# Optimization experiments

Measured on AMD Instinct MI355X. Metric: run time of the kernel, lower is better.

Reference implementation:

```python
import jax, jax.numpy as jnp
import numpy as np

EPS_RMS = 1e-6   # assumed eps for utils.rms
EPS_LN = 1e-5    # matches F.layer_norm eps in LayerNorm


def rmsnorm(z):
    # utils.rms: normalize to unit RMS over the channel dim
    return z * jax.lax.rsqrt(jnp.mean(jnp.square(z), axis=-1, keepdims=True) + EPS_RMS)


def layernorm(x, w):
    mu = jnp.mean(x, axis=-1, keepdims=True)
    var = jnp.var(x, axis=-1, keepdims=True)
    return (x - mu) * jax.lax.rsqrt(var + EPS_LN) * w


def polar_orthogonal(W):
    # utils.fast_polar_decomposition: orthogonal factor of polar decomposition
    U, _, Vh = jnp.linalg.svd(W, full_matrices=False)
    return U @ Vh


def pscan2(q, P1, P2, identity):
    # Hillis-Steele inclusive parallel scan over the time axis with combine
    # scan(left, right) = rms(left @ P1^T + right @ P2^T); positions with no
    # left operand at a level keep their current value (identity pads the shift).
    B, T, C = q.shape
    d = 1
    while d < T:
        left = jnp.concatenate(
            [jnp.broadcast_to(identity, (B, d, C)), q[:, : T - d]], axis=1)
        z = rmsnorm(jnp.einsum('btc,dc->btd', left, P1)
                    + jnp.einsum('btc,dc->btd', q, P2))
        upd = (jnp.arange(T) >= d)[None, :, None]
        q = jnp.where(upd, z, q)
        d *= 2
    return q


def setup_inputs() -> dict:
    key = jax.random.key(0)
    ks = jax.random.split(key, 9)
    B, T, C = 4, 4096, 512
    inv = 1.0 / np.sqrt(C)
    return {
        'x': jax.random.normal(ks[0], (B, T, C), jnp.float32),
        'ln1_w': jnp.ones((C,), jnp.float32),
        'Wq': jax.random.normal(ks[1], (C, C), jnp.float32) * inv,
        'Wv': jax.random.normal(ks[2], (C, C), jnp.float32) * inv,
        'Wo': jax.random.normal(ks[3], (C, C), jnp.float32) * inv,
        'identity': jax.random.uniform(ks[4], (C,), jnp.float32),
        'Wp1': jax.random.normal(ks[5], (C, C), jnp.float32),
        'Wp2': jax.random.normal(ks[6], (C, C), jnp.float32),
        'ln2_w': jnp.ones((C,), jnp.float32),
        'Wfc': jax.random.normal(ks[7], (4 * C, C), jnp.float32) * inv,
        'Wpr': jax.random.normal(ks[8], (C, 4 * C), jnp.float32) * (1.0 / np.sqrt(4 * C)),
    }


def reference(x, ln1_w, Wq, Wv, Wo, identity, Wp1, Wp2, ln2_w, Wfc, Wpr):
    # SSM branch (dropout = 0 in eval)
    h = layernorm(x, ln1_w)
    q = h @ Wq.T
    v = h @ Wv.T
    P1 = polar_orthogonal(Wp1)
    P2 = polar_orthogonal(Wp2)
    q = pscan2(q, P1, P2, identity)
    x = x + (q * v) @ Wo.T
    # MLP branch
    h2 = layernorm(x, ln2_w)
    h2 = jax.nn.gelu(h2 @ Wfc.T, approximate=False)  # torch nn.GELU() is exact erf
    x = x + h2 @ Wpr.T
    return x
```

## Files before the change

kernel.cpp:

```cpp
#include <hip/hip_runtime.h>
#include <hip/hip_bf16.h>

typedef __hip_bfloat16 bf16;
typedef __attribute__((ext_vector_type(8))) short short8;
typedef __attribute__((ext_vector_type(4))) short short4v;
typedef __attribute__((ext_vector_type(4))) float f32x4;

#define DEVINL static __device__ __forceinline__

DEVINL float b2f(bf16 x) { return __bfloat162float(x); }
DEVINL bf16 f2b(float x) { return __float2bfloat16(x); }
DEVINL float sb2f(short s) { return b2f(__builtin_bit_cast(bf16, s)); }
DEVINL short f2sb(float x) { return __builtin_bit_cast(short, f2b(x)); }

DEVINL void gload16(const void* g, void* l) {
  __builtin_amdgcn_global_load_lds(
      (const __attribute__((address_space(1))) void*)g,
      (__attribute__((address_space(3))) void*)l, 16, 0, 0);
}

DEVINL float wave_sum(float v) {
#pragma unroll
  for (int o = 32; o > 0; o >>= 1) v += __shfl_down(v, o, 64);
  return v;
}

DEVINL float wave_allsum(float v) {
#pragma unroll
  for (int o = 32; o > 0; o >>= 1) v += __shfl_xor(v, o, 64);
  return v;
}

#define BARRIER()                             \
  do {                                        \
    __asm__ __volatile__("" ::: "memory");    \
    __builtin_amdgcn_s_barrier();             \
    __asm__ __volatile__("" ::: "memory");    \
  } while (0)
#define WAIT_LGKM0() __asm__ __volatile__("s_waitcnt lgkmcnt(0)" ::: "memory")
#define WAIT_VM(n) __asm__ __volatile__("s_waitcnt vmcnt(" #n ")" ::: "memory")

template <int MODE, bool SPLIT, int BM>
__global__ __launch_bounds__(256) void gemm_nt(
    const bf16* __restrict__ A0, const bf16* __restrict__ A1,
    const bf16* __restrict__ B0, const bf16* __restrict__ B1,
    int K, int lda, int ldb, long bsA, long bsB, long bsC,
    bf16* __restrict__ outb, int ldo,
    const float* __restrict__ resf, float* __restrict__ outf,
    float alpha, float beta, float* __restrict__ Xf,
    bf16* __restrict__ Whi, bf16* __restrict__ Wlo,
    bf16* __restrict__ Thi, bf16* __restrict__ Tlo) {
  constexpr int BK = 64;
  constexpr int MT = BM / 32;
  constexpr int NLOAD = BM * BK / 2048;
  extern __shared__ char smem[];
  bf16* AsH = (bf16*)smem;
  bf16* BsH = AsH + BM * BK;
  bf16* AsL = BsH + BM * BK;
  bf16* BsL = AsL + BM * BK;

  const int t = threadIdx.x;
  const int lane = t & 63, w = t >> 6;
  const long bz = blockIdx.z;
  const bf16* Ab0 = A0 + bz * bsA;
  const bf16* Bb0 = B0 + bz * bsB;
  const bf16* Ab1 = SPLIT ? (A1 + bz * bsA) : nullptr;
  const bf16* Bb1 = SPLIT ? (B1 + bz * bsB) : nullptr;

  const int row0 = blockIdx.x * BM, col0 = blockIdx.y * BM;
  const int wm = (w >> 1) * (BM / 2), wn = (w & 1) * (BM / 2);
  const int jj = lane >> 4, r16 = lane & 15;

  f32x4 acc[MT][MT] = {};

  for (int k0 = 0; k0 < K; k0 += BK) {
    __syncthreads();
#pragma unroll
    for (int s = 0; s < NLOAD; ++s) {
      const int L = s * 256 + t;
      const int cj = L / BM, m = L % BM;
      const long ga = (long)(row0 + m) * lda + (k0 + cj * 8);
      const long gb = (long)(col0 + m) * ldb + (k0 + cj * 8);
      gload16(Ab0 + ga, AsH + L * 8);
      gload16(Bb0 + gb, BsH + L * 8);
      if (SPLIT) {
        gload16(Ab1 + ga, AsL + L * 8);
        gload16(Bb1 + gb, BsL + L * 8);
      }
    }
    __syncthreads();

#pragma unroll
    for (int kk = 0; kk < BK / 32; ++kk) {
      short8 a[MT], b[MT], al[MT], bl[MT];
#pragma unroll
      for (int mt = 0; mt < MT; ++mt) {
        const int o = (kk * 4 + jj) * BM * 8 + (wm + mt * 16 + r16) * 8;
        a[mt] = *(const short8*)(AsH + o);
        if (SPLIT) al[mt] = *(const short8*)(AsL + o);
      }
#pragma unroll
      for (int nt = 0; nt < MT; ++nt) {
        const int o = (kk * 4 + jj) * BM * 8 + (wn + nt * 16 + r16) * 8;
        b[nt] = *(const short8*)(BsH + o);
        if (SPLIT) bl[nt] = *(const short8*)(BsL + o);
      }
#pragma unroll
      for (int mt = 0; mt < MT; ++mt)
#pragma unroll
        for (int nt = 0; nt < MT; ++nt) {
          acc[mt][nt] = __builtin_amdgcn_mfma_f32_16x16x32_bf16(a[mt], b[nt], acc[mt][nt], 0, 0, 0);
          if (SPLIT) {
            acc[mt][nt] = __builtin_amdgcn_mfma_f32_16x16x32_bf16(a[mt], bl[nt], acc[mt][nt], 0, 0, 0);
            acc[mt][nt] = __builtin_amdgcn_mfma_f32_16x16x32_bf16(al[mt], b[nt], acc[mt][nt], 0, 0, 0);
          }
        }
    }
  }

#pragma unroll
  for (int mt = 0; mt < MT; ++mt)
#pragma unroll
    for (int nt = 0; nt < MT; ++nt)
#pragma unroll
      for (int r = 0; r < 4; ++r) {
        const int row = row0 + wm + mt * 16 + jj * 4 + r;
        const int col = col0 + wn + nt * 16 + r16;
        const float v = acc[mt][nt][r];
        if (MODE == 3) {
          const long i = bz * bsC + (long)row * 512 + col;
          const bf16 h = f2b(v);
          Whi[i] = h;
          Wlo[i] = f2b(v - b2f(h));
        } else if (MODE == 4) {
          const long i = bz * bsC + (long)row * 512 + col;
          const float nv = alpha * Xf[i] + beta * v;
          Xf[i] = nv;
          const bf16 h = f2b(nv);
          const bf16 l = f2b(nv - b2f(h));
          Whi[i] = h; Wlo[i] = l;
          const long it2 = bz * bsC + (long)col * 512 + row;
          Thi[it2] = h; Tlo[it2] = l;
        }
      }
}

DEVINL void loadA4(const bf16* p, short8 (&dst)[4][2]) {
#pragma unroll
  for (int mf = 0; mf < 4; ++mf)
#pragma unroll
    for (int kk = 0; kk < 2; ++kk)
      dst[mf][kk] = *(const short8*)(p + kk * 4096 + mf * 128);
}
DEVINL void loadB2(const bf16* p, short8 (&dst)[2][2]) {
#pragma unroll
  for (int nf = 0; nf < 2; ++nf)
#pragma unroll
    for (int kk = 0; kk < 2; ++kk)
      dst[nf][kk] = *(const short8*)(p + kk * 4096 + nf * 128);
}
template <int QM, int QN>
DEVINL void mfma16(const short8 (&af)[4][2], const short8 (&bb)[2][2],
                   f32x4 (&acc)[8][4]) {
  __builtin_amdgcn_s_setprio(1);
#pragma unroll
  for (int mf = 0; mf < 4; ++mf)
#pragma unroll
    for (int nf = 0; nf < 2; ++nf)
#pragma unroll
      for (int kk = 0; kk < 2; ++kk)
        acc[QM * 4 + mf][QN * 2 + nf] = __builtin_amdgcn_mfma_f32_16x16x32_bf16(
            af[mf][kk], bb[nf][kk], acc[QM * 4 + mf][QN * 2 + nf], 0, 0, 0);
  __builtin_amdgcn_s_setprio(0);
}

template <int MODE, bool PSCAN>
__global__ __launch_bounds__(512, 2) void gemm256(
    const bf16* __restrict__ A, const bf16* __restrict__ B, int K, int lda,
    int ldb, bf16* __restrict__ outb, int ldo, const float* __restrict__ resf,
    float* __restrict__ outf, int d, int start, int nyb) {
  extern __shared__ char smem[];
  const int t = threadIdx.x;
  const int lane = t & 63;
  const int w = t >> 6, wr = w >> 2, wc = w & 3;
  const int jj = lane >> 4, r16 = lane & 15;
  const int sm = t & 127, cj = t >> 7;

  int row0, batch0 = 0;
  if (PSCAN) {
    const int b = blockIdx.x / nyb;
    const int ty = blockIdx.x - b * nyb;
    batch0 = b * 4096;
    row0 = batch0 + start + ty * 256;
  } else {
    row0 = blockIdx.x * 256;
  }
  const int col0 = blockIdx.y * 256;

  auto slotp = [&](int buf, int mat, int half) -> bf16* {
    return (bf16*)(smem + (((buf << 2) | (mat << 1) | half) << 14));
  };
  auto stageA = [&](int buf, int half, int kt) {
    bf16* dst = slotp(buf, 0, half) + t * 8;
    long ga;
    if (PSCAN) {
      const int rr = row0 + half * 128 + sm;
      if (kt < 8) {
        int rs = rr - d;
        if (rs < batch0) rs = batch0;
        ga = (long)rs * 1024 + kt * 64 + cj * 8;
      } else {
        ga = (long)rr * 1024 + (kt - 8) * 64 + cj * 8;
      }
    } else {
      ga = (long)(row0 + half * 128 + sm) * lda + kt * 64 + cj * 8;
    }
    gload16(A + ga, dst);
    gload16(A + ga + 32, dst + 4096);
  };
  auto stageB = [&](int buf, int half, int kt) {
    bf16* dst = slotp(buf, 1, half) + t * 8;
    const long gb = (long)(col0 + half * 128 + sm) * ldb + kt * 64 + cj * 8;
    gload16(B + gb, dst);
    gload16(B + gb + 32, dst + 4096);
  };

  const int aBase = (jj * 128 + wr * 64 + r16) * 8;
  const int bBase = (jj * 128 + wc * 32 + r16) * 8;
  f32x4 acc[8][4] = {};

  const int nit = K >> 7;

  stageA(0, 0, 0); stageB(0, 0, 0); stageB(0, 1, 0); stageA(0, 1, 0);
  stageA(1, 0, 1); stageB(1, 1, 1);
  WAIT_VM(4);
  BARRIER();

  for (int it = 0; it < nit; ++it) {
    const int k1 = 2 * it + 1, k2 = 2 * it + 2, k3 = 2 * it + 3;
    const bool more = (it + 1 < nit);
    short8 af[4][2], b0[2][2], b1[2][2];
    loadA4(slotp(0, 0, 0) + aBase, af);
    loadB2(slotp(0, 1, 0) + bBase, b0);
    stageA(1, 1, k1);
    BARRIER(); WAIT_LGKM0();
    mfma16<0, 0>(af, b0, acc);
    BARRIER();
    loadB2(slotp(0, 1, 1) + bBase, b1);
    stageB(1, 0, k1);
    BARRIER(); WAIT_LGKM0();
    mfma16<0, 1>(af, b1, acc);
    BARRIER();
    loadA4(slotp(0, 0, 1) + aBase, af);
    if (more) stageA(0, 0, k2);
    BARRIER(); WAIT_LGKM0();
    mfma16<1, 1>(af, b1, acc);
    BARRIER();
    if (more) stageB(0, 1, k2);
    BARRIER(); WAIT_LGKM0();
    mfma16<1, 0>(af, b0, acc);
    if (more) { WAIT_VM(4); } else { WAIT_VM(0); }
    BARRIER();
    loadA4(slotp(1, 0, 0) + aBase, af);
    loadB2(slotp(1, 1, 0) + bBase, b0);
    if (more) stageA(0, 1, k2);
    BARRIER(); WAIT_LGKM0();
    mfma16<0, 0>(af, b0, acc);
    BARRIER();
    loadB2(slotp(1, 1, 1) + bBase, b1);
    if (more) stageB(0, 0, k2);
    BARRIER(); WAIT_LGKM0();
    mfma16<0, 1>(af, b1, acc);
    BARRIER();
    loadA4(slotp(1, 0, 1) + aBase, af);
    if (more) stageA(1, 0, k3);
    BARRIER(); WAIT_LGKM0();
    mfma16<1, 1>(af, b1, acc);
    BARRIER();
    if (more) stageB(1, 1, k3);
    BARRIER(); WAIT_LGKM0();
    mfma16<1, 0>(af, b0, acc);
    if (more) WAIT_VM(4);
    BARRIER();
  }

  if (MODE == 2) {
#pragma unroll
    for (int q = 0; q < 8; ++q)
#pragma unroll
      for (int n = 0; n < 4; ++n)
#pragma unroll
        for (int r = 0; r < 4; ++r) {
          const int row = row0 + (q >> 2) * 128 + wr * 64 + (q & 3) * 16 + jj * 4 + r;
          const int col = col0 + (n >> 1) * 128 + wc * 32 + (n & 1) * 16 + r16;
          const long i = (long)row * ldo + col;
          outf[i] = resf[i] + acc[q][n][r];
        }
    return;
  }

  __syncthreads();
  bf16* Cs = (bf16*)smem;
#pragma unroll
  for (int q = 0; q < 8; ++q)
#pragma unroll
    for (int n = 0; n < 4; ++n)
#pragma unroll
      for (int r = 0; r < 4; ++r) {
        const int row = (q >> 2) * 128 + wr * 64 + (q & 3) * 16 + jj * 4 + r;
        const int col = (n >> 1) * 128 + wc * 32 + (n & 1) * 16 + r16;
        float v = acc[q][n][r];
        if (MODE == 1) v = 0.5f * v * (1.0f + erff(v * 0.70710678118654752f));
        Cs[row * 256 + col] = f2b(v);
      }
  __syncthreads();
#pragma unroll
  for (int i = 0; i < 16; ++i) {
    const int rr = i * 16 + (t >> 5);
    const int cc = (t & 31) * 8;
    *(short8*)(outb + (long)(row0 + rr) * ldo + (col0 + cc)) =
        *(const short8*)(Cs + rr * 256 + cc);
  }
}

__global__ __launch_bounds__(256) void repack_pcat(const bf16* __restrict__ Xhi,
                                                   bf16* __restrict__ Pcat) {
  const int e = (blockIdx.x * 256 + threadIdx.x) << 3;
  const int c = e >> 10, k = e & 1023;
  const bf16* src = (k < 512) ? (Xhi + (long)c * 512 + k)
                              : (Xhi + 262144 + (long)c * 512 + (k - 512));
  *(short8*)(Pcat + e) = *(const short8*)src;
}

__global__ __launch_bounds__(256) void fnorm(const float* __restrict__ W1,
                                             const float* __restrict__ W2,
                                             float* __restrict__ sigsq) {
  const int b = blockIdx.x >> 8;
  const float4 v = *(const float4*)((b ? W2 : W1) +
                                    (((long)(blockIdx.x & 255) * 256 + threadIdx.x) << 2));
  float s = v.x * v.x + v.y * v.y + v.z * v.z + v.w * v.w;
  s = wave_sum(s);
  if ((threadIdx.x & 63) == 0) atomicAdd(&sigsq[b], s);
}

__global__ __launch_bounds__(256) void scale_init(
    const float* __restrict__ W1, const float* __restrict__ W2,
    const float* __restrict__ sigsq, float* __restrict__ Xf,
    bf16* __restrict__ Xhi, bf16* __restrict__ Xlo,
    bf16* __restrict__ Thi, bf16* __restrict__ Tlo) {
  const long idx = (long)blockIdx.x * 256 + threadIdx.x;
  const int b = (int)(idx >> 18);
  const int i = (int)(idx & 262143);
  const float s = rsqrtf(sigsq[b]);
  const float val = (b ? W2[i] : W1[i]) * s;
  const long o = ((long)b << 18) + i;
  Xf[o] = val;
  const bf16 h = f2b(val);
  const bf16 l = f2b(val - b2f(h));
  Xhi[o] = h; Xlo[o] = l;
  const int r = i >> 9, c = i & 511;
  const long ot = ((long)b << 18) + (long)c * 512 + r;
  Thi[ot] = h; Tlo[ot] = l;
}

__global__ __launch_bounds__(256) void convert_weights(
    const float* __restrict__ Wq, const float* __restrict__ Wv,
    const float* __restrict__ Wo, const float* __restrict__ Wfc,
    const float* __restrict__ Wpr, bf16* __restrict__ Wqvb,
    bf16* __restrict__ Wob, bf16* __restrict__ Wfcb, bf16* __restrict__ Wprb) {
  const long e = ((long)blockIdx.x * 256 + threadIdx.x) << 2;
  const float* src; bf16* dst; long off;
  if (e < 262144)       { src = Wq;  dst = Wqvb;          off = e; }
  else if (e < 524288)  { src = Wv;  dst = Wqvb + 262144; off = e - 262144; }
  else if (e < 786432)  { src = Wo;  dst = Wob;           off = e - 524288; }
  else if (e < 1835008) { src = Wfc; dst = Wfcb;          off = e - 786432; }
  else                  { src = Wpr; dst = Wprb;          off = e - 1835008; }
  const float4 v = *(const float4*)(src + off);
  short4v o4;
  o4[0] = f2sb(v.x); o4[1] = f2sb(v.y); o4[2] = f2sb(v.z); o4[3] = f2sb(v.w);
  *(short4v*)(dst + off) = o4;
}

__global__ __launch_bounds__(256) void ln_rows(const float* __restrict__ x,
                                               const float* __restrict__ w,
                                               bf16* __restrict__ out) {
  const int row = (blockIdx.x << 2) + (threadIdx.x >> 6);
  const int lane = threadIdx.x & 63;
  const float* xr = x + (long)row * 512 + lane * 8;
  const float4 a = *(const float4*)xr;
  const float4 b = *(const float4*)(xr + 4);
  float v[8] = {a.x, a.y, a.z, a.w, b.x, b.y, b.z, b.w};
  float s1 = 0.f, s2 = 0.f;
#pragma unroll
  for (int i = 0; i < 8; ++i) { s1 += v[i]; s2 += v[i] * v[i]; }
  s1 = wave_allsum(s1);
  s2 = wave_allsum(s2);
  const float mean = s1 * (1.0f / 512.0f);
  const float var = s2 * (1.0f / 512.0f) - mean * mean;
  const float inv = rsqrtf(var + 1e-5f);
  const float4 w1 = *(const float4*)(w + lane * 8);
  const float4 w2 = *(const float4*)(w + lane * 8 + 4);
  const float wv[8] = {w1.x, w1.y, w1.z, w1.w, w2.x, w2.y, w2.z, w2.w};
  short8 o8;
#pragma unroll
  for (int i = 0; i < 8; ++i) o8[i] = f2sb((v[i] - mean) * inv * wv[i]);
  *(short8*)(out + (long)row * 512 + lane * 8) = o8;
}

__global__ __launch_bounds__(256) void pscan_combine(const bf16* __restrict__ S,
                                                     bf16* __restrict__ QV, int d) {
  const int span = 4096 - d;
  const int wid = (blockIdx.x << 2) + (threadIdx.x >> 6);
  const int lane = threadIdx.x & 63;
  const int b = wid / span;
  const int tt = d + (wid - b * span);
  const long rowQ = (long)b * 4096 + tt;
  const short8 s8 = *(const short8*)(S + rowQ * 512 + lane * 8);
  float s[8]; float ss = 0.f;
#pragma unroll
  for (int i = 0; i < 8; ++i) {
    const float v = sb2f(s8[i]);
    s[i] = v; ss += v * v;
  }
  ss = wave_allsum(ss);
  const float inv = rsqrtf(ss * (1.0f / 512.0f) + 1e-6f);
  short8 o8;
#pragma unroll
  for (int i = 0; i < 8; ++i) o8[i] = f2sb(s[i] * inv);
  *(short8*)(QV + rowQ * 1024 + lane * 8) = o8;
}

__global__ __launch_bounds__(256) void qv_mul(const bf16* __restrict__ QV,
                                              bf16* __restrict__ u) {
  const long base = ((long)blockIdx.x * 256 + threadIdx.x) << 3;
  const long row = base >> 9;
  const int c = (int)(base & 511);
  const short8 q8 = *(const short8*)(QV + row * 1024 + c);
  const short8 v8 = *(const short8*)(QV + row * 1024 + 512 + c);
  short8 o8;
#pragma unroll
  for (int i = 0; i < 8; ++i) o8[i] = f2sb(sb2f(q8[i]) * sb2f(v8[i]));
  *(short8*)(u + row * 512 + c) = o8;
}

extern "C" void kernel_launch(void* const* d_in, const int* in_sizes, int n_in,
                              void* d_out, int out_size, void* d_ws, size_t ws_size,
                              hipStream_t stream) {
  (void)in_sizes; (void)n_in; (void)out_size; (void)ws_size;
  const float* x    = (const float*)d_in[0];
  const float* ln1w = (const float*)d_in[1];
  const float* Wq   = (const float*)d_in[2];
  const float* Wv   = (const float*)d_in[3];
  const float* Wo   = (const float*)d_in[4];
  const float* Wp1  = (const float*)d_in[6];
  const float* Wp2  = (const float*)d_in[7];
  const float* ln2w = (const float*)d_in[8];
  const float* Wfc  = (const float*)d_in[9];
  const float* Wpr  = (const float*)d_in[10];
  float* out = (float*)d_out;

  const long M = 16384;
  char* ws = (char*)d_ws;
  size_t off = 0;
  auto alloc = [&](size_t bytes) -> void* {
    void* p = ws + off;
    off += (bytes + 255) & ~(size_t)255;
    return p;
  };
  bf16* YZ   = (bf16*)alloc(M * 1024 * 2);
  bf16* QV   = (bf16*)alloc(M * 1024 * 2);
  bf16* hb   = (bf16*)alloc(M * 512 * 2);
  bf16* Wqvb = (bf16*)alloc(1024 * 512 * 2);
  bf16* Wob  = (bf16*)alloc(512 * 512 * 2);
  bf16* Wfcb = (bf16*)alloc(2048 * 512 * 2);
  bf16* Wprb = (bf16*)alloc(512 * 2048 * 2);
  float* Xf  = (float*)alloc(2 * 262144 * 4);
  bf16* Xhi  = (bf16*)alloc(2 * 262144 * 2);
  bf16* Xlo  = (bf16*)alloc(2 * 262144 * 2);
  bf16* XtAh = (bf16*)alloc(2 * 262144 * 2);
  bf16* XtAl = (bf16*)alloc(2 * 262144 * 2);
  bf16* XtBh = (bf16*)alloc(2 * 262144 * 2);
  bf16* XtBl = (bf16*)alloc(2 * 262144 * 2);
  bf16* Ghi  = (bf16*)alloc(2 * 262144 * 2);
  bf16* Glo  = (bf16*)alloc(2 * 262144 * 2);
  bf16* Pcat = (bf16*)alloc(512 * 1024 * 2);
  float* sig = (float*)alloc(256);
  bf16* S  = YZ;
  bf16* h3 = YZ;

  const auto Z0 = nullptr;

  hipMemsetAsync(sig, 0, 2 * sizeof(float), stream);
  fnorm<<<512, 256, 0, stream>>>(Wp1, Wp2, sig);
  scale_init<<<2048, 256, 0, stream>>>(Wp1, Wp2, sig, Xf, Xhi, Xlo, XtAh, XtAl);

  bf16 *tch = XtAh, *tcl = XtAl, *tnh = XtBh, *tnl = XtBl;
  const long Sz = 262144;
  for (int i = 0; i < 20; ++i) {
    const bool pol = (i >= 16);
    const float ac = pol ? 1.5f : 2.0f;
    const float bc = pol ? -0.5f : -1.0f;
    dim3 g(8, 8, 2);
    gemm_nt<3, true, 64><<<g, 256, 32768, stream>>>(
        Xhi, Xlo, Xhi, Xlo, 512, 512, 512, Sz, Sz, Sz,
        Z0, 0, Z0, Z0, 0.f, 0.f, Z0, Ghi, Glo, Z0, Z0);
    gemm_nt<4, true, 64><<<g, 256, 32768, stream>>>(
        Ghi, Glo, tch, tcl, 512, 512, 512, Sz, Sz, Sz,
        Z0, 0, Z0, Z0, ac, bc, Xf, Xhi, Xlo, tnh, tnl);
    bf16* sw;
    sw = tch; tch = tnh; tnh = sw;
    sw = tcl; tcl = tnl; tnl = sw;
  }
  repack_pcat<<<256, 256, 0, stream>>>(Xhi, Pcat);

  convert_weights<<<2816, 256, 0, stream>>>(Wq, Wv, Wo, Wfc, Wpr, Wqvb, Wob, Wfcb, Wprb);

  ln_rows<<<4096, 256, 0, stream>>>(x, ln1w, hb);
  gemm256<0, false><<<dim3(64, 4), 512, 131072, stream>>>(
      hb, Wqvb, 512, 512, 512, QV, 1024, Z0, Z0, 0, 0, 0);

  for (int d = 1; d < 4096; d <<= 1) {
    const int start = d & ~255;
    const int nyb = (4096 - start) >> 8;
    gemm256<0, true><<<dim3(4 * nyb, 2), 512, 131072, stream>>>(
        QV, Pcat, 1024, 1024, 1024, S, 512, Z0, Z0, d, start, nyb);
    pscan_combine<<<4096 - d, 256, 0, stream>>>(S, QV, d);
  }

  qv_mul<<<4096, 256, 0, stream>>>(QV, hb);
  gemm256<2, false><<<dim3(64, 2), 512, 131072, stream>>>(
      hb, Wob, 512, 512, 512, Z0, 512, x, out, 0, 0, 0);

  ln_rows<<<4096, 256, 0, stream>>>(out, ln2w, hb);
  gemm256<1, false><<<dim3(64, 8), 512, 131072, stream>>>(
      hb, Wfcb, 512, 512, 512, h3, 2048, Z0, Z0, 0, 0, 0);
  gemm256<2, false><<<dim3(64, 2), 512, 131072, stream>>>(
      h3, Wprb, 2048, 2048, 2048, Z0, 512, out, out, 0, 0, 0);
}
```

Measured before the change: 1.608 ms.

## Restructure pscan GEMM to full-row projection and add BN=128 residual GEMM path

Each scan step now multiplies every QV row (the q half, K=512) by [P1;P2] stacked as a 1024x512 matrix, instead of gathering shifted rows over K=1024. The shift and sum move into the combine kernel, which reads row t-d from the first half of Y and row t from the second half. This drops the Pcat repack and the start-offset row skipping, so every step computes all 4096 rows per batch. Separately, the residual-output GEMMs get a BN=128 variant with a 3-stage pipeline that fills more blocks, and the main loop drops several barriers. All of this adds wasted work on early scan steps and changes the sync ordering.

After: 1.454 ms. 1.11x faster.

```diff
diff --git a/kernel.cpp b/kernel.cpp
--- a/kernel.cpp
+++ b/kernel.cpp
@@ -45,8 +45,6 @@
     const bf16* __restrict__ A0, const bf16* __restrict__ A1,
     const bf16* __restrict__ B0, const bf16* __restrict__ B1,
     int K, int lda, int ldb, long bsA, long bsB, long bsC,
-    bf16* __restrict__ outb, int ldo,
-    const float* __restrict__ resf, float* __restrict__ outf,
     float alpha, float beta, float* __restrict__ Xf,
     bf16* __restrict__ Whi, bf16* __restrict__ Wlo,
     bf16* __restrict__ Thi, bf16* __restrict__ Tlo) {
@@ -173,12 +171,26 @@
             af[mf][kk], bb[nf][kk], acc[QM * 4 + mf][QN * 2 + nf], 0, 0, 0);
   __builtin_amdgcn_s_setprio(0);
 }
-
-template <int MODE, bool PSCAN>
+template <int QM>
+DEVINL void mfma16h(const short8 (&af)[4][2], const short8 (&bb)[2][2],
+                    f32x4 (&acc)[8][2]) {
+  __builtin_amdgcn_s_setprio(1);
+#pragma unroll
+  for (int mf = 0; mf < 4; ++mf)
+#pragma unroll
+    for (int nf = 0; nf < 2; ++nf)
+#pragma unroll
+      for (int kk = 0; kk < 2; ++kk)
+        acc[QM * 4 + mf][nf] = __builtin_amdgcn_mfma_f32_16x16x32_bf16(
+            af[mf][kk], bb[nf][kk], acc[QM * 4 + mf][nf], 0, 0, 0);
+  __builtin_amdgcn_s_setprio(0);
+}
+
+template <int MODE, int BN>
 __global__ __launch_bounds__(512, 2) void gemm256(
     const bf16* __restrict__ A, const bf16* __restrict__ B, int K, int lda,
     int ldb, bf16* __restrict__ outb, int ldo, const float* __restrict__ resf,
-    float* __restrict__ outf, int d, int start, int nyb) {
+    float* __restrict__ outf) {
   extern __shared__ char smem[];
   const int t = threadIdx.x;
   const int lane = t & 63;
@@ -186,150 +198,172 @@
   const int jj = lane >> 4, r16 = lane & 15;
   const int sm = t & 127, cj = t >> 7;
 
-  int row0, batch0 = 0;
-  if (PSCAN) {
-    const int b = blockIdx.x / nyb;
-    const int ty = blockIdx.x - b * nyb;
-    batch0 = b * 4096;
-    row0 = batch0 + start + ty * 256;
-  } else {
-    row0 = blockIdx.x * 256;
-  }
-  const int col0 = blockIdx.y * 256;
-
-  auto slotp = [&](int buf, int mat, int half) -> bf16* {
-    return (bf16*)(smem + (((buf << 2) | (mat << 1) | half) << 14));
-  };
-  auto stageA = [&](int buf, int half, int kt) {
-    bf16* dst = slotp(buf, 0, half) + t * 8;
-    long ga;
-    if (PSCAN) {
-      const int rr = row0 + half * 128 + sm;
-      if (kt < 8) {
-        int rs = rr - d;
-        if (rs < batch0) rs = batch0;
-        ga = (long)rs * 1024 + kt * 64 + cj * 8;
-      } else {
-        ga = (long)rr * 1024 + (kt - 8) * 64 + cj * 8;
-      }
-    } else {
-      ga = (long)(row0 + half * 128 + sm) * lda + kt * 64 + cj * 8;
-    }
-    gload16(A + ga, dst);
-    gload16(A + ga + 32, dst + 4096);
-  };
-  auto stageB = [&](int buf, int half, int kt) {
-    bf16* dst = slotp(buf, 1, half) + t * 8;
-    const long gb = (long)(col0 + half * 128 + sm) * ldb + kt * 64 + cj * 8;
-    gload16(B + gb, dst);
-    gload16(B + gb + 32, dst + 4096);
-  };
+  const int row0 = blockIdx.x * 256;
+  const int col0 = blockIdx.y * BN;
 
   const int aBase = (jj * 128 + wr * 64 + r16) * 8;
   const int bBase = (jj * 128 + wc * 32 + r16) * 8;
-  f32x4 acc[8][4] = {};
-
-  const int nit = K >> 7;
-
-  stageA(0, 0, 0); stageB(0, 0, 0); stageB(0, 1, 0); stageA(0, 1, 0);
-  stageA(1, 0, 1); stageB(1, 1, 1);
-  WAIT_VM(4);
-  BARRIER();
-
-  for (int it = 0; it < nit; ++it) {
-    const int k1 = 2 * it + 1, k2 = 2 * it + 2, k3 = 2 * it + 3;
-    const bool more = (it + 1 < nit);
-    short8 af[4][2], b0[2][2], b1[2][2];
-    loadA4(slotp(0, 0, 0) + aBase, af);
-    loadB2(slotp(0, 1, 0) + bBase, b0);
-    stageA(1, 1, k1);
-    BARRIER(); WAIT_LGKM0();
-    mfma16<0, 0>(af, b0, acc);
+
+  if constexpr (BN == 256) {
+    auto slotp = [&](int buf, int mat, int half) -> bf16* {
+      return (bf16*)(smem + (((buf << 2) | (mat << 1) | half) << 14));
+    };
+    auto stageA = [&](int buf, int half, int kt) {
+      bf16* dst = slotp(buf, 0, half) + t * 8;
+      const long ga = (long)(row0 + half * 128 + sm) * lda + kt * 64 + cj * 8;
+      gload16(A + ga, dst);
+      gload16(A + ga + 32, dst + 4096);
+    };
+    auto stageB = [&](int buf, int half, int kt) {
+      bf16* dst = slotp(buf, 1, half) + t * 8;
+      const long gb = (long)(col0 + half * 128 + sm) * ldb + kt * 64 + cj * 8;
+      gload16(B + gb, dst);
+      gload16(B + gb + 32, dst + 4096);
+    };
+
+    f32x4 acc[8][4] = {};
+    const int nit = K >> 7;
+
+    stageA(0, 0, 0); stageB(0, 0, 0); stageB(0, 1, 0); stageA(0, 1, 0);
+    stageA(1, 0, 1); stageB(1, 1, 1);
+    WAIT_VM(4);
     BARRIER();
-    loadB2(slotp(0, 1, 1) + bBase, b1);
-    stageB(1, 0, k1);
-    BARRIER(); WAIT_LGKM0();
-    mfma16<0, 1>(af, b1, acc);
+
+    for (int it = 0; it < nit; ++it) {
+      const int k1 = 2 * it + 1, k2 = 2 * it + 2, k3 = 2 * it + 3;
+      const bool more = (it + 1 < nit);
+      short8 af[4][2], b0[2][2], b1[2][2];
+      loadA4(slotp(0, 0, 0) + aBase, af);
+      loadB2(slotp(0, 1, 0) + bBase, b0);
+      stageA(1, 1, k1);
+      BARRIER(); WAIT_LGKM0();
+      mfma16<0, 0>(af, b0, acc);
+      loadB2(slotp(0, 1, 1) + bBase, b1);
+      stageB(1, 0, k1);
+      BARRIER(); WAIT_LGKM0();
+      mfma16<0, 1>(af, b1, acc);
+      loadA4(slotp(0, 0, 1) + aBase, af);
+      if (more) stageA(0, 0, k2);
+      BARRIER(); WAIT_LGKM0();
+      mfma16<1, 1>(af, b1, acc);
+      if (more) stageB(0, 1, k2);
+      if (more) { WAIT_VM(4); } else { WAIT_VM(0); }
+      BARRIER();
+      mfma16<1, 0>(af, b0, acc);
+      loadA4(slotp(1, 0, 0) + aBase, af);
+      loadB2(slotp(1, 1, 0) + bBase, b0);
+      if (more) stageA(0, 1, k2);
+      BARRIER(); WAIT_LGKM0();
+      mfma16<0, 0>(af, b0, acc);
+      loadB2(slotp(1, 1, 1) + bBase, b1);
+      if (more) stageB(0, 0, k2);
+      BARRIER(); WAIT_LGKM0();
+      mfma16<0, 1>(af, b1, acc);
+      loadA4(slotp(1, 0, 1) + aBase, af);
+      if (more) stageA(1, 0, k3);
+      BARRIER(); WAIT_LGKM0();
+      mfma16<1, 1>(af, b1, acc);
+      if (more) stageB(1, 1, k3);
+      if (more) WAIT_VM(4);
+      BARRIER();
+      mfma16<1, 0>(af, b0, acc);
+    }
+
+    if constexpr (MODE == 2) {
+#pragma unroll
+      for (int q = 0; q < 8; ++q)
+#pragma unroll
+        for (int n = 0; n < 4; ++n)
+#pragma unroll
+          for (int r = 0; r < 4; ++r) {
+            const int row = row0 + (q >> 2) * 128 + wr * 64 + (q & 3) * 16 + jj * 4 + r;
+            const int col = col0 + (n >> 1) * 128 + wc * 32 + (n & 1) * 16 + r16;
+            const long i = (long)row * ldo + col;
+            outf[i] = resf[i] + acc[q][n][r];
+          }
+      return;
+    } else {
+      __syncthreads();
+      bf16* Cs = (bf16*)smem;
+#pragma unroll
+      for (int q = 0; q < 8; ++q)
+#pragma unroll
+        for (int n = 0; n < 4; ++n)
+#pragma unroll
+          for (int r = 0; r < 4; ++r) {
+            const int row = (q >> 2) * 128 + wr * 64 + (q & 3) * 16 + jj * 4 + r;
+            const int col = (n >> 1) * 128 + wc * 32 + (n & 1) * 16 + r16;
+            float v = acc[q][n][r];
+            if (MODE == 1) v = 0.5f * v * (1.0f + erff(v * 0.70710678118654752f));
+            Cs[row * 256 + col] = f2b(v);
+          }
+      __syncthreads();
+#pragma unroll
+      for (int i = 0; i < 16; ++i) {
+        const int rr = i * 16 + (t >> 5);
+        const int cc = (t & 31) * 8;
+        *(short8*)(outb + (long)(row0 + rr) * ldo + (col0 + cc)) =
+            *(const short8*)(Cs + rr * 256 + cc);
+      }
+    }
+  } else {
+    auto slotp3 = [&](int buf, int slot) -> bf16* {
+      return (bf16*)(smem + ((buf * 3 + slot) << 14));
+    };
+    auto stage3A = [&](int buf, int half, int kt) {
+      bf16* dst = slotp3(buf, half) + t * 8;
+      const long ga = (long)(row0 + half * 128 + sm) * lda + kt * 64 + cj * 8;
+      gload16(A + ga, dst);
+      gload16(A + ga + 32, dst + 4096);
+    };
+    auto stage3B = [&](int buf, int kt) {
+      bf16* dst = slotp3(buf, 2) + t * 8;
+      const long gb = (long)(col0 + sm) * ldb + kt * 64 + cj * 8;
+      gload16(B + gb, dst);
+      gload16(B + gb + 32, dst + 4096);
+    };
+
+    f32x4 acc[8][2] = {};
+    const int nt = K >> 6;
+
+    stage3A(0, 0, 0); stage3A(0, 1, 0); stage3B(0, 0);
+    stage3A(1, 0, 1); stage3A(1, 1, 1); stage3B(1, 1);
+    WAIT_VM(6);
     BARRIER();
-    loadA4(slotp(0, 0, 1) + aBase, af);
-    if (more) stageA(0, 0, k2);
-    BARRIER(); WAIT_LGKM0();
-    mfma16<1, 1>(af, b1, acc);
-    BARRIER();
-    if (more) stageB(0, 1, k2);
-    BARRIER(); WAIT_LGKM0();
-    mfma16<1, 0>(af, b0, acc);
-    if (more) { WAIT_VM(4); } else { WAIT_VM(0); }
-    BARRIER();
-    loadA4(slotp(1, 0, 0) + aBase, af);
-    loadB2(slotp(1, 1, 0) + bBase, b0);
-    if (more) stageA(0, 1, k2);
-    BARRIER(); WAIT_LGKM0();
-    mfma16<0, 0>(af, b0, acc);
-    BARRIER();
-    loadB2(slotp(1, 1, 1) + bBase, b1);
-    if (more) stageB(0, 0, k2);
-    BARRIER(); WAIT_LGKM0();
-    mfma16<0, 1>(af, b1, acc);
-    BARRIER();
-    loadA4(slotp(1, 0, 1) + aBase, af);
-    if (more) stageA(1, 0, k3);
-    BARRIER(); WAIT_LGKM0();
-    mfma16<1, 1>(af, b1, acc);
-    BARRIER();
-    if (more) stageB(1, 1, k3);
-    BARRIER(); WAIT_LGKM0();
-    mfma16<1, 0>(af, b0, acc);
-    if (more) WAIT_VM(4);
-    BARRIER();
-  }
-
-  if (MODE == 2) {
+
+    int cb = 0;
+    for (int tk = 0; tk < nt; ++tk) {
+      int sb = cb + 2; if (sb >= 3) sb -= 3;
+      const bool more = (tk + 2 < nt);
+      short8 af[4][2], bb2[2][2];
+      bf16* sA0 = slotp3(cb, 0);
+      bf16* sA1 = slotp3(cb, 1);
+      bf16* sB = slotp3(cb, 2);
+      loadA4(sA0 + aBase, af);
+      loadB2(sB + bBase, bb2);
+      if (more) { stage3A(sb, 0, tk + 2); stage3B(sb, tk + 2); }
+      BARRIER(); WAIT_LGKM0();
+      mfma16h<0>(af, bb2, acc);
+      loadA4(sA1 + aBase, af);
+      if (more) stage3A(sb, 1, tk + 2);
+      if (more) { WAIT_VM(6); } else { WAIT_VM(0); }
+      BARRIER(); WAIT_LGKM0();
+      mfma16h<1>(af, bb2, acc);
+      cb = (cb + 1 == 3) ? 0 : cb + 1;
+    }
+
 #pragma unroll
     for (int q = 0; q < 8; ++q)
 #pragma unroll
-      for (int n = 0; n < 4; ++n)
+      for (int n = 0; n < 2; ++n)
 #pragma unroll
         for (int r = 0; r < 4; ++r) {
           const int row = row0 + (q >> 2) * 128 + wr * 64 + (q & 3) * 16 + jj * 4 + r;
-          const int col = col0 + (n >> 1) * 128 + wc * 32 + (n & 1) * 16 + r16;
+          const int col = col0 + wc * 32 + n * 16 + r16;
           const long i = (long)row * ldo + col;
           outf[i] = resf[i] + acc[q][n][r];
         }
-    return;
   }
-
-  __syncthreads();
-  bf16* Cs = (bf16*)smem;
-#pragma unroll
-  for (int q = 0; q < 8; ++q)
-#pragma unroll
-    for (int n = 0; n < 4; ++n)
-#pragma unroll
-      for (int r = 0; r < 4; ++r) {
-        const int row = (q >> 2) * 128 + wr * 64 + (q & 3) * 16 + jj * 4 + r;
-        const int col = (n >> 1) * 128 + wc * 32 + (n & 1) * 16 + r16;
-        float v = acc[q][n][r];
-        if (MODE == 1) v = 0.5f * v * (1.0f + erff(v * 0.70710678118654752f));
-        Cs[row * 256 + col] = f2b(v);
-      }
-  __syncthreads();
-#pragma unroll
-  for (int i = 0; i < 16; ++i) {
-    const int rr = i * 16 + (t >> 5);
-    const int cc = (t & 31) * 8;
-    *(short8*)(outb + (long)(row0 + rr) * ldo + (col0 + cc)) =
-        *(const short8*)(Cs + rr * 256 + cc);
-  }
-}
-
-__global__ __launch_bounds__(256) void repack_pcat(const bf16* __restrict__ Xhi,
-                                                   bf16* __restrict__ Pcat) {
-  const int e = (blockIdx.x * 256 + threadIdx.x) << 3;
-  const int c = e >> 10, k = e & 1023;
-  const bf16* src = (k < 512) ? (Xhi + (long)c * 512 + k)
-                              : (Xhi + 262144 + (long)c * 512 + (k - 512));
-  *(short8*)(Pcat + e) = *(const short8*)src;
 }
 
 __global__ __launch_bounds__(256) void fnorm(const float* __restrict__ W1,
@@ -407,19 +441,21 @@
   *(short8*)(out + (long)row * 512 + lane * 8) = o8;
 }
 
-__global__ __launch_bounds__(256) void pscan_combine(const bf16* __restrict__ S,
-                                                     bf16* __restrict__ QV, int d) {
+__global__ __launch_bounds__(256) void pscan_combine2(const bf16* __restrict__ Y,
+                                                      bf16* __restrict__ QV, int d) {
   const int span = 4096 - d;
   const int wid = (blockIdx.x << 2) + (threadIdx.x >> 6);
   const int lane = threadIdx.x & 63;
   const int b = wid / span;
   const int tt = d + (wid - b * span);
-  const long rowQ = (long)b * 4096 + tt;
-  const short8 s8 = *(const short8*)(S + rowQ * 512 + lane * 8);
+  const long row2 = (long)b * 4096 + tt;
+  const long row1 = row2 - d;
+  const short8 a8 = *(const short8*)(Y + row1 * 1024 + lane * 8);
+  const short8 b8 = *(const short8*)(Y + row2 * 1024 + 512 + lane * 8);
   float s[8]; float ss = 0.f;
 #pragma unroll
   for (int i = 0; i < 8; ++i) {
-    const float v = sb2f(s8[i]);
+    const float v = sb2f(a8[i]) + sb2f(b8[i]);
     s[i] = v; ss += v * v;
   }
   ss = wave_allsum(ss);
@@ -427,7 +463,7 @@
   short8 o8;
 #pragma unroll
   for (int i = 0; i < 8; ++i) o8[i] = f2sb(s[i] * inv);
-  *(short8*)(QV + rowQ * 1024 + lane * 8) = o8;
+  *(short8*)(QV + row2 * 1024 + lane * 8) = o8;
 }
 
 __global__ __launch_bounds__(256) void qv_mul(const bf16* __restrict__ QV,
@@ -483,9 +519,8 @@
   bf16* XtBl = (bf16*)alloc(2 * 262144 * 2);
   bf16* Ghi  = (bf16*)alloc(2 * 262144 * 2);
   bf16* Glo  = (bf16*)alloc(2 * 262144 * 2);
-  bf16* Pcat = (bf16*)alloc(512 * 1024 * 2);
   float* sig = (float*)alloc(256);
-  bf16* S  = YZ;
+  bf16* Y  = YZ;
   bf16* h3 = YZ;
 
   const auto Z0 = nullptr;
@@ -503,37 +538,34 @@
     dim3 g(8, 8, 2);
     gemm_nt<3, true, 64><<<g, 256, 32768, stream>>>(
         Xhi, Xlo, Xhi, Xlo, 512, 512, 512, Sz, Sz, Sz,
-        Z0, 0, Z0, Z0, 0.f, 0.f, Z0, Ghi, Glo, Z0, Z0);
+        0.f, 0.f, Z0, Ghi, Glo, Z0, Z0);
     gemm_nt<4, true, 64><<<g, 256, 32768, stream>>>(
         Ghi, Glo, tch, tcl, 512, 512, 512, Sz, Sz, Sz,
-        Z0, 0, Z0, Z0, ac, bc, Xf, Xhi, Xlo, tnh, tnl);
+        ac, bc, Xf, Xhi, Xlo, tnh, tnl);
     bf16* sw;
     sw = tch; tch = tnh; tnh = sw;
     sw = tcl; tcl = tnl; tnl = sw;
   }
-  repack_pcat<<<256, 256, 0, stream>>>(Xhi, Pcat);
 
   convert_weights<<<2816, 256, 0, stream>>>(Wq, Wv, Wo, Wfc, Wpr, Wqvb, Wob, Wfcb, Wprb);
 
   ln_rows<<<4096, 256, 0, stream>>>(x, ln1w, hb);
-  gemm256<0, false><<<dim3(64, 4), 512, 131072, stream>>>(
-      hb, Wqvb, 512, 512, 512, QV, 1024, Z0, Z0, 0, 0, 0);
+  gemm256<0, 256><<<dim3(64, 4), 512, 131072, stream>>>(
+      hb, Wqvb, 512, 512, 512, QV, 1024, Z0, Z0);
 
   for (int d = 1; d < 4096; d <<= 1) {
-    const int start = d & ~255;
-    const int nyb = (4096 - start) >> 8;
-    gemm256<0, true><<<dim3(4 * nyb, 2), 512, 131072, stream>>>(
-        QV, Pcat, 1024, 1024, 1024, S, 512, Z0, Z0, d, start, nyb);
-    pscan_combine<<<4096 - d, 256, 0, stream>>>(S, QV, d);
+    gemm256<0, 256><<<dim3(64, 4), 512, 131072, stream>>>(
+        QV, Xhi, 512, 1024, 512, Y, 1024, Z0, Z0);
+    pscan_combine2<<<4096 - d, 256, 0, stream>>>(Y, QV, d);
   }
 
   qv_mul<<<4096, 256, 0, stream>>>(QV, hb);
-  gemm256<2, false><<<dim3(64, 2), 512, 131072, stream>>>(
-      hb, Wob, 512, 512, 512, Z0, 512, x, out, 0, 0, 0);
+  gemm256<2, 128><<<dim3(64, 4), 512, 147456, stream>>>(
+      hb, Wob, 512, 512, 512, Z0, 512, x, out);
 
   ln_rows<<<4096, 256, 0, stream>>>(out, ln2w, hb);
-  gemm256<1, false><<<dim3(64, 8), 512, 131072, stream>>>(
-      hb, Wfcb, 512, 512, 512, h3, 2048, Z0, Z0, 0, 0, 0);
-  gemm256<2, false><<<dim3(64, 2), 512, 131072, stream>>>(
-      h3, Wprb, 2048, 2048, 2048, Z0, 512, out, out, 0, 0, 0);
-}
+  gemm256<1, 256><<<dim3(64, 8), 512, 131072, stream>>>(
+      hb, Wfcb, 512, 512, 512, h3, 2048, Z0, Z0);
+  gemm256<2, 128><<<dim3(64, 4), 512, 147456, stream>>>(
+      h3, Wprb, 2048, 2048, 2048, Z0, 512, out, out);
+}
```
